# Kernel optimization log

Measured on AMD Instinct MI355X. Metric: run time of the kernel, lower is better.

## Reference

```python
import jax, jax.numpy as jnp
import numpy as np

B = 1024           # number of drug pairs (graphs per side)
ATOMS = 64         # atoms per molecule
N = B * ATOMS      # total atoms per side
H = 512            # hidden_size * number_of_molecules
FFN_H = 2048
OUT = 86           # num_tasks


def setup_inputs() -> dict:
    key = jax.random.key(0)
    ks = jax.random.split(key, 12)
    inv = 1.0 / np.sqrt(H)
    inv2 = 1.0 / np.sqrt(2 * H)
    invf = 1.0 / np.sqrt(FFN_H)
    return {
        "left_output": jax.random.normal(ks[0], (B, H), jnp.float32),
        "right_output": jax.random.normal(ks[1], (B, H), jnp.float32),
        "left_atom": jax.random.normal(ks[2], (N, H), jnp.float32),
        "right_atom": jax.random.normal(ks[3], (N, H), jnp.float32),
        "left_batch": jnp.arange(N, dtype=jnp.int32) // ATOMS,
        "right_batch": jnp.arange(N, dtype=jnp.int32) // ATOMS,
        "noise": jax.random.uniform(ks[4], (B, H), jnp.float32),
        "w_i_w": jax.random.normal(ks[5], (H, H), jnp.float32) * inv,
        "w_i_b": jnp.zeros((H,), jnp.float32),
        "prj_i_w": jax.random.normal(ks[6], (H, H), jnp.float32) * inv,
        "prj_i_b": jnp.zeros((H,), jnp.float32),
        "ffn1_w": jax.random.normal(ks[7], (2 * H, FFN_H), jnp.float32) * inv2,
        "ffn1_b": jnp.zeros((FFN_H,), jnp.float32),
        "ffn2_w": jax.random.normal(ks[8], (FFN_H, OUT), jnp.float32) * invf,
        "ffn2_b": jnp.zeros((OUT,), jnp.float32),
    }


def _seg_softmax(s, seg, num_segments):
    m = jax.ops.segment_max(s, seg, num_segments=num_segments)
    e = jnp.exp(s - m[seg])
    z = jax.ops.segment_sum(e, seg, num_segments=num_segments)
    return e / z[seg]


def reference(left_output, right_output, left_atom, right_atom,
              left_batch, right_batch, noise,
              w_i_w, w_i_b, prj_i_w, prj_i_b,
              ffn1_w, ffn1_b, ffn2_w, ffn2_b):
    # repeat_interleave(left_output, degree(right_batch)) == gather by segment id
    left_align = left_output[right_batch]    # [N_r, H]
    right_align = right_output[left_batch]   # [N_l, H]

    # cross-molecule coattention scores (elementwise product + reduce)
    left_scores = jnp.sum((left_atom @ w_i_w + w_i_b) * (right_align @ prj_i_w + prj_i_b), axis=-1)
    left_scores = _seg_softmax(left_scores, left_batch, B)
    right_scores = jnp.sum((right_atom @ w_i_w + w_i_b) * (left_align @ prj_i_w + prj_i_b), axis=-1)
    right_scores = _seg_softmax(right_scores, right_batch, B)

    # attention-weighted global add pool
    h_output = jax.ops.segment_sum(left_atom * right_align * left_scores[:, None], left_batch, num_segments=B)
    t_output = jax.ops.segment_sum(right_atom * left_align * right_scores[:, None], right_batch, num_segments=B)

    # sign-directed noise perturbation (same noise for both sides, as in original)
    nrm = jnp.maximum(jnp.linalg.norm(noise, axis=-1, keepdims=True), 1e-12)
    noise_n = noise / nrm
    h_pert = h_output + jnp.sign(h_output) * noise_n * 0.1
    t_pert = t_output + jnp.sign(t_output) * noise_n * 0.1

    pair = jnp.concatenate([h_pert, t_pert], axis=-1)  # [B, 2H]
    hid = jax.nn.relu(pair @ ffn1_w + ffn1_b)
    output = hid @ ffn2_w + ffn2_b  # training mode: raw logits, no sigmoid
    return (output, h_output, h_pert, left_scores, right_scores, left_output, right_output)
```

## Files before the change

### kernel.cpp

```cpp
#include <hip/hip_runtime.h>
#include <hip/hip_bf16.h>
#include <float.h>

#define B_ 1024
#define H_ 512
#define N_ (B_ * 64)
#define FFN_ 2048
#define OUT_ 86

typedef __bf16 bf16_t;
typedef __attribute__((ext_vector_type(8))) __bf16 bf16x8;
typedef __attribute__((ext_vector_type(4))) float f32x4;

__device__ __forceinline__ float wred_sum(float v) {
#pragma unroll
  for (int m = 32; m; m >>= 1) v += __shfl_xor(v, m);
  return v;
}

__device__ __forceinline__ void gload_lds16(const void* g, void* l) {
  __builtin_amdgcn_global_load_lds((const __attribute__((address_space(1))) unsigned int*)g,
                                   (__attribute__((address_space(3))) unsigned int*)l, 16, 0, 0);
}

template <bool BT, bool BIAS>
__global__ __launch_bounds__(256) void gemm64(const float* __restrict__ A1, const float* __restrict__ A2,
                                              int M1, const float* __restrict__ Bm,
                                              const float* __restrict__ bias, float* __restrict__ C,
                                              int N, int K) {
  __shared__ float As[16][68];
  __shared__ float Bs[16][68];
  const int bm = blockIdx.x * 64, bn = blockIdx.y * 64;
  const float* __restrict__ A = (bm < M1) ? (A1 + (size_t)bm * K) : (A2 + (size_t)(bm - M1) * K);
  const int t = threadIdx.x;
  const int tx = t & 15, ty = t >> 4;
  float acc[4][4] = {};
  for (int k0 = 0; k0 < K; k0 += 16) {
#pragma unroll
    for (int i = 0; i < 4; i++) {
      int m = (t >> 4) + i * 16;
      As[t & 15][m] = A[(size_t)m * K + k0 + (t & 15)];
    }
    if (BT) {
#pragma unroll
      for (int i = 0; i < 4; i++) {
        int n = (t >> 4) + i * 16;
        Bs[t & 15][n] = Bm[(size_t)(bn + n) * K + k0 + (t & 15)];
      }
    } else {
#pragma unroll
      for (int i = 0; i < 4; i++) {
        int kk = (t >> 6) + i * 4;
        Bs[kk][t & 63] = Bm[(size_t)(k0 + kk) * N + bn + (t & 63)];
      }
    }
    __syncthreads();
#pragma unroll
    for (int kk = 0; kk < 16; kk++) {
      float4 av = *(const float4*)&As[kk][ty * 4];
      float4 bv = *(const float4*)&Bs[kk][tx * 4];
      float a_[4] = {av.x, av.y, av.z, av.w};
      float b_[4] = {bv.x, bv.y, bv.z, bv.w};
#pragma unroll
      for (int i = 0; i < 4; i++)
#pragma unroll
        for (int j = 0; j < 4; j++) acc[i][j] += a_[i] * b_[j];
    }
    __syncthreads();
  }
#pragma unroll
  for (int i = 0; i < 4; i++) {
    int m = bm + ty * 4 + i;
    float tmp[4];
#pragma unroll
    for (int j = 0; j < 4; j++) {
      float x = acc[i][j];
      if (BIAS) x += bias[bn + tx * 4 + j];
      tmp[j] = x;
    }
    float4 v;
    v.x = tmp[0]; v.y = tmp[1]; v.z = tmp[2]; v.w = tmp[3];
    *(float4*)&C[(size_t)m * N + bn + tx * 4] = v;
  }
}

__global__ __launch_bounds__(256) void k_atoms6(const float* __restrict__ atomL, const float* __restrict__ atomR,
                                                const float* __restrict__ uLR,
                                                float* __restrict__ scoresL, float* __restrict__ scoresR,
                                                float* __restrict__ pL, float* __restrict__ pR) {
  const int pair = blockIdx.x;
  const int side = pair >> 10, b = pair & 1023;
  const int t = threadIdx.x, wave = t >> 6, lane = t & 63;

  __shared__ __align__(16) float sbuf[4][2][2][512];
  __shared__ float s_raw[64];
  __shared__ float mz[4][2];

  const float* __restrict__ atom = side ? atomR : atomL;
  const float* __restrict__ u = uLR + (size_t)pair * H_;
  float ur[8];
  *(f32x4*)&ur[0] = *(const f32x4*)&u[lane * 4];
  *(f32x4*)&ur[4] = *(const f32x4*)&u[256 + lane * 4];

  const char* gbase = (const char*)(atom + ((size_t)b * 64 + wave * 16) * H_);

  {
    char* lb = (char*)&sbuf[wave][0][0][0];
    gload_lds16(gbase + lane * 16, lb + lane * 16);
    gload_lds16(gbase + 1024 + lane * 16, lb + 1024 + lane * 16);
    gload_lds16(gbase + 2048 + lane * 16, lb + 2048 + lane * 16);
    gload_lds16(gbase + 3072 + lane * 16, lb + 3072 + lane * 16);
  }

  float q[8] = {};
  float m_run = -FLT_MAX, z_run = 0.f, myraw = 0.f;

#pragma unroll
  for (int c = 0; c < 8; c++) {
    if (c < 7) {
      const char* gb = gbase + (size_t)(c + 1) * 4096;
      char* lb = (char*)&sbuf[wave][(c + 1) & 1][0][0];
      gload_lds16(gb + lane * 16, lb + lane * 16);
      gload_lds16(gb + 1024 + lane * 16, lb + 1024 + lane * 16);
      gload_lds16(gb + 2048 + lane * 16, lb + 2048 + lane * 16);
      gload_lds16(gb + 3072 + lane * 16, lb + 3072 + lane * 16);
      asm volatile("s_waitcnt vmcnt(4)" ::: "memory");
    } else {
      asm volatile("s_waitcnt vmcnt(0)" ::: "memory");
    }
    __builtin_amdgcn_sched_barrier(0);
    const float* bc = &sbuf[wave][c & 1][0][0];
    float a0[8], a1[8];
    *(f32x4*)&a0[0] = *(const f32x4*)(bc + lane * 4);
    *(f32x4*)&a0[4] = *(const f32x4*)(bc + 256 + lane * 4);
    *(f32x4*)&a1[0] = *(const f32x4*)(bc + 512 + lane * 4);
    *(f32x4*)&a1[4] = *(const f32x4*)(bc + 512 + 256 + lane * 4);
    float d0 = 0.f, d1 = 0.f;
#pragma unroll
    for (int j = 0; j < 8; j++) { d0 += a0[j] * ur[j]; d1 += a1[j] * ur[j]; }
    d0 = wred_sum(d0);
    d1 = wred_sum(d1);
    myraw = (lane == wave * 16 + c * 2) ? d0 : myraw;
    myraw = (lane == wave * 16 + c * 2 + 1) ? d1 : myraw;
    float m_new = fmaxf(m_run, fmaxf(d0, d1));
    float r = __expf(m_run - m_new);
    float e0 = __expf(d0 - m_new), e1 = __expf(d1 - m_new);
    z_run = z_run * r + e0 + e1;
    m_run = m_new;
#pragma unroll
    for (int j = 0; j < 8; j++) q[j] = q[j] * r + e0 * a0[j] + e1 * a1[j];
  }

  if (lane == 0) { mz[wave][0] = m_run; mz[wave][1] = z_run; }
  if ((lane >> 4) == wave) s_raw[lane] = myraw;
  __syncthreads();

  const float M = fmaxf(fmaxf(mz[0][0], mz[1][0]), fmaxf(mz[2][0], mz[3][0]));
  const float Z = mz[0][1] * __expf(mz[0][0] - M) + mz[1][1] * __expf(mz[1][0] - M) +
                  mz[2][1] * __expf(mz[2][0] - M) + mz[3][1] * __expf(mz[3][0] - M);
  const float zinv = 1.f / Z;
  const float f = __expf(m_run - M);

  float* pp = &sbuf[0][0][0][0];
  f32x4 q0 = {q[0] * f, q[1] * f, q[2] * f, q[3] * f};
  f32x4 q1 = {q[4] * f, q[5] * f, q[6] * f, q[7] * f};
  *(f32x4*)&pp[wave * 512 + lane * 4] = q0;
  *(f32x4*)&pp[wave * 512 + 256 + lane * 4] = q1;
  __syncthreads();

  float v0 = (pp[t] + pp[512 + t] + pp[1024 + t] + pp[1536 + t]) * zinv;
  float v1 = (pp[t + 256] + pp[512 + t + 256] + pp[1024 + t + 256] + pp[1536 + t + 256]) * zinv;
  float* p = (side ? pR : pL) + (size_t)b * H_;
  p[t] = v0;
  p[t + 256] = v1;
  if (t < 64) (side ? scoresR : scoresL)[(size_t)b * 64 + t] = __expf(s_raw[t] - M) * zinv;
}

__global__ __launch_bounds__(512) void k_pert(const float* __restrict__ lo, const float* __restrict__ ro,
                                              const float* __restrict__ noise,
                                              const float* __restrict__ pL, const float* __restrict__ pR,
                                              float* __restrict__ h_out, float* __restrict__ h_pert,
                                              bf16_t* __restrict__ pairbf) {
  const int b = blockIdx.x, t = threadIdx.x;
  float nv = noise[(size_t)b * H_ + t];
  float sq = nv * nv;
  sq = wred_sum(sq);
  __shared__ float red[8];
  if ((t & 63) == 0) red[t >> 6] = sq;
  __syncthreads();
  float tot = 0.f;
#pragma unroll
  for (int i = 0; i < 8; i++) tot += red[i];
  float nrm = fmaxf(sqrtf(tot), 1e-12f);
  float nn = nv / nrm * 0.1f;
  float h = ro[(size_t)b * H_ + t] * pL[(size_t)b * H_ + t];
  float tt = lo[(size_t)b * H_ + t] * pR[(size_t)b * H_ + t];
  float sh = (h > 0.f) ? 1.f : ((h < 0.f) ? -1.f : 0.f);
  float st = (tt > 0.f) ? 1.f : ((tt < 0.f) ? -1.f : 0.f);
  float hp = h + sh * nn;
  float tp = tt + st * nn;
  h_out[(size_t)b * H_ + t] = h;
  h_pert[(size_t)b * H_ + t] = hp;
  pairbf[(size_t)b * 1024 + t] = (bf16_t)hp;
  pairbf[(size_t)b * 1024 + 512 + t] = (bf16_t)tp;
}

__global__ __launch_bounds__(256) void k_w1t(const float* __restrict__ W1, bf16_t* __restrict__ W1t) {
  __shared__ float tile[32][33];
  const int bx = blockIdx.x;
  const int by = blockIdx.y;
  const int tx = threadIdx.x & 31, ty = threadIdx.x >> 5;
#pragma unroll
  for (int i = ty; i < 32; i += 8)
    tile[i][tx] = W1[(size_t)(by * 32 + i) * FFN_ + bx * 32 + tx];
  __syncthreads();
#pragma unroll
  for (int i = ty; i < 32; i += 8)
    W1t[(size_t)(bx * 32 + i) * 1024 + by * 32 + tx] = (bf16_t)tile[tx][i];
}

__global__ __launch_bounds__(256) void k_ffn1(const bf16_t* __restrict__ Abf, const bf16_t* __restrict__ Bt,
                                              const float* __restrict__ bias, float* __restrict__ C) {
  __shared__ bf16_t As[64 * 64];
  __shared__ bf16_t Bs[64 * 64];
  const int bm = blockIdx.x * 64, bn = blockIdx.y * 64;
  const int t = threadIdx.x;
  const int lane = t & 63, wave = t >> 6;
  const int wm = wave & 1, wn = wave >> 1;
  const int l15 = lane & 15, l4 = lane >> 4;
  f32x4 acc[2][2] = {{{0.f, 0.f, 0.f, 0.f}, {0.f, 0.f, 0.f, 0.f}},
                     {{0.f, 0.f, 0.f, 0.f}, {0.f, 0.f, 0.f, 0.f}}};

  for (int k0 = 0; k0 < 1024; k0 += 64) {
#pragma unroll
    for (int r = 0; r < 2; r++) {
      const int off = (r * 256 + t) * 16;
      const int row = off >> 7;
      const int g = (off >> 4) & 7;
      const int scb = ((g ^ (row & 7)) << 4);
      gload_lds16((const char*)Abf + (size_t)(bm + row) * 2048 + k0 * 2 + scb, (char*)As + off);
      gload_lds16((const char*)Bt + (size_t)(bn + row) * 2048 + k0 * 2 + scb, (char*)Bs + off);
    }
    __syncthreads();
#pragma unroll
    for (int ks = 0; ks < 2; ks++) {
      const int ar0 = wm * 32 + l15, ar1 = ar0 + 16;
      const int br0 = wn * 32 + l15, br1 = br0 + 16;
      const int gA = ks * 4 + l4;
      bf16x8 a0 = *(const bf16x8*)((const char*)As + ar0 * 128 + ((gA ^ (ar0 & 7)) << 4));
      bf16x8 a1 = *(const bf16x8*)((const char*)As + ar1 * 128 + ((gA ^ (ar1 & 7)) << 4));
      bf16x8 b0 = *(const bf16x8*)((const char*)Bs + br0 * 128 + ((gA ^ (br0 & 7)) << 4));
      bf16x8 b1 = *(const bf16x8*)((const char*)Bs + br1 * 128 + ((gA ^ (br1 & 7)) << 4));
      acc[0][0] = __builtin_amdgcn_mfma_f32_16x16x32_bf16(a0, b0, acc[0][0], 0, 0, 0);
      acc[0][1] = __builtin_amdgcn_mfma_f32_16x16x32_bf16(a0, b1, acc[0][1], 0, 0, 0);
      acc[1][0] = __builtin_amdgcn_mfma_f32_16x16x32_bf16(a1, b0, acc[1][0], 0, 0, 0);
      acc[1][1] = __builtin_amdgcn_mfma_f32_16x16x32_bf16(a1, b1, acc[1][1], 0, 0, 0);
    }
    __syncthreads();
  }
#pragma unroll
  for (int mi = 0; mi < 2; mi++)
#pragma unroll
    for (int nj = 0; nj < 2; nj++)
#pragma unroll
      for (int r = 0; r < 4; r++) {
        const int m = bm + wm * 32 + mi * 16 + l4 * 4 + r;
        const int n = bn + wn * 32 + nj * 16 + l15;
        float v = acc[mi][nj][r] + bias[n];
        C[(size_t)m * FFN_ + n] = fmaxf(v, 0.f);
      }
}

__global__ void k_w2t(const float* __restrict__ W2, float* __restrict__ W2t) {
  int idx = blockIdx.x * 256 + threadIdx.x;
  if (idx < OUT_ * FFN_) {
    int n = idx / FFN_, k = idx % FFN_;
    W2t[idx] = W2[(size_t)k * OUT_ + n];
  }
}

__global__ __launch_bounds__(256) void k_ffn2(const float* __restrict__ hid, const float* __restrict__ W2t,
                                              const float* __restrict__ b2, float* __restrict__ out) {
  const int b0 = blockIdx.x * 2;
  const int t = threadIdx.x, wave = t >> 6, lane = t & 63;
  float4 h0[8], h1[8];
  const float* r0 = hid + (size_t)b0 * FFN_;
#pragma unroll
  for (int j = 0; j < 8; j++) {
    h0[j] = *(const float4*)&r0[lane * 4 + j * 256];
    h1[j] = *(const float4*)&r0[FFN_ + lane * 4 + j * 256];
  }
  for (int n = wave; n < OUT_; n += 4) {
    const float* wrow = W2t + (size_t)n * FFN_;
    float s0 = 0.f, s1 = 0.f;
#pragma unroll
    for (int j = 0; j < 8; j++) {
      float4 w4 = *(const float4*)&wrow[lane * 4 + j * 256];
      s0 += w4.x * h0[j].x + w4.y * h0[j].y + w4.z * h0[j].z + w4.w * h0[j].w;
      s1 += w4.x * h1[j].x + w4.y * h1[j].y + w4.z * h1[j].z + w4.w * h1[j].w;
    }
    s0 = wred_sum(s0);
    s1 = wred_sum(s1);
    if (lane == 0) {
      out[(size_t)b0 * OUT_ + n] = s0 + b2[n];
      out[(size_t)(b0 + 1) * OUT_ + n] = s1 + b2[n];
    }
  }
}

extern "C" void kernel_launch(void* const* d_in, const int* in_sizes, int n_in,
                              void* d_out, int out_size, void* d_ws, size_t ws_size,
                              hipStream_t stream) {
  const float* lo = (const float*)d_in[0];
  const float* ro = (const float*)d_in[1];
  const float* la = (const float*)d_in[2];
  const float* ra = (const float*)d_in[3];
  const float* noise = (const float*)d_in[6];
  const float* w_i_w = (const float*)d_in[7];
  const float* prj_w = (const float*)d_in[9];
  const float* prj_b = (const float*)d_in[10];
  const float* W1 = (const float*)d_in[11];
  const float* b1 = (const float*)d_in[12];
  const float* W2 = (const float*)d_in[13];
  const float* b2 = (const float*)d_in[14];

  float* out = (float*)d_out;
  float* o_logits = out;
  float* o_hout  = out + 88064;
  float* o_hpert = o_hout + 524288;
  float* o_ls    = o_hpert + 524288;
  float* o_rs    = o_ls + 65536;
  float* o_lo    = o_rs + 65536;
  float* o_ro    = o_lo + 524288;

  float* ws = (float*)d_ws;
  float* T    = ws; ws += 2048 * 512;
  float* uLR  = ws; ws += 2048 * 512;
  float* pL   = ws; ws += B_ * H_;
  float* pR   = ws; ws += B_ * H_;
  float* hid  = ws; ws += B_ * FFN_;
  float* W2t  = ws; ws += OUT_ * FFN_;
  bf16_t* pairbf = (bf16_t*)ws; ws += B_ * 1024 / 2;
  bf16_t* W1t    = (bf16_t*)ws; ws += FFN_ * 1024 / 2;

  gemm64<false, true><<<dim3(32, 8), 256, 0, stream>>>(ro, lo, 1024, prj_w, prj_b, T, 512, 512);
  gemm64<true, false><<<dim3(32, 8), 256, 0, stream>>>(T, T, 1 << 30, w_i_w, nullptr, uLR, 512, 512);
  k_w1t<<<dim3(64, 32), 256, 0, stream>>>(W1, W1t);
  k_atoms6<<<2048, 256, 0, stream>>>(la, ra, uLR, o_ls, o_rs, pL, pR);
  k_pert<<<1024, 512, 0, stream>>>(lo, ro, noise, pL, pR, o_hout, o_hpert, pairbf);
  k_ffn1<<<dim3(16, 32), 256, 0, stream>>>(pairbf, W1t, b1, hid);
  k_w2t<<<688, 256, 0, stream>>>(W2, W2t);
  k_ffn2<<<512, 256, 0, stream>>>(hid, W2t, b2, o_logits);
  hipMemcpyAsync(o_lo, lo, (size_t)B_ * H_ * 4, hipMemcpyDeviceToDevice, stream);
  hipMemcpyAsync(o_ro, ro, (size_t)B_ * H_ * 4, hipMemcpyDeviceToDevice, stream);
}
```

Before: 164.8 us.

## Precompute combined weight matrix and rewrite atom attention as two-pass kernel

The projection chain is reassociated: a 512x512 matrix from w_i_w and prj_w plus a bias vector is built once, and the pooled outputs are then multiplied by it in a single GEMM. This replaces two 1024-row GEMMs and drops the T buffer. The atom kernel is also rewritten. It no longer streams atoms through LDS with an online softmax. Instead it computes all 64 scores with direct global loads, runs a block-wide softmax, and then reads the atoms a second time to form the weighted sum. That second read doubles atom traffic, though the rows for a molecule may still be in cache.

New measurement: 200.1 us. 1.21x slower.

```diff
diff --git a/kernel.cpp b/kernel.cpp
--- a/kernel.cpp
+++ b/kernel.cpp
@@ -17,10 +17,24 @@
   for (int m = 32; m; m >>= 1) v += __shfl_xor(v, m);
   return v;
 }
+__device__ __forceinline__ float wred_max(float v) {
+#pragma unroll
+  for (int m = 32; m; m >>= 1) v = fmaxf(v, __shfl_xor(v, m));
+  return v;
+}
 
 __device__ __forceinline__ void gload_lds16(const void* g, void* l) {
   __builtin_amdgcn_global_load_lds((const __attribute__((address_space(1))) unsigned int*)g,
                                    (__attribute__((address_space(3))) unsigned int*)l, 16, 0, 0);
+}
+
+__global__ void k_prep(const float* __restrict__ w_i_w, const float* __restrict__ prj_b,
+                       float* __restrict__ dv) {
+  int k = blockIdx.x, l = threadIdx.x;
+  float s = 0.f;
+  for (int h = l; h < H_; h += 64) s += w_i_w[k * H_ + h] * prj_b[h];
+  s = wred_sum(s);
+  if (l == 0) dv[k] = s;
 }
 
 template <bool BT, bool BIAS>
@@ -84,7 +98,7 @@
   }
 }
 
-__global__ __launch_bounds__(256) void k_atoms6(const float* __restrict__ atomL, const float* __restrict__ atomR,
+__global__ __launch_bounds__(256) void k_atoms8(const float* __restrict__ atomL, const float* __restrict__ atomR,
                                                 const float* __restrict__ uLR,
                                                 float* __restrict__ scoresL, float* __restrict__ scoresR,
                                                 float* __restrict__ pL, float* __restrict__ pR) {
@@ -92,88 +106,56 @@
   const int side = pair >> 10, b = pair & 1023;
   const int t = threadIdx.x, wave = t >> 6, lane = t & 63;
 
-  __shared__ __align__(16) float sbuf[4][2][2][512];
-  __shared__ float s_raw[64];
-  __shared__ float mz[4][2];
+  __shared__ float s_all[64];
+  __shared__ float s_nrm[64];
 
   const float* __restrict__ atom = side ? atomR : atomL;
   const float* __restrict__ u = uLR + (size_t)pair * H_;
-  float ur[8];
-  *(f32x4*)&ur[0] = *(const f32x4*)&u[lane * 4];
-  *(f32x4*)&ur[4] = *(const f32x4*)&u[256 + lane * 4];
-
-  const char* gbase = (const char*)(atom + ((size_t)b * 64 + wave * 16) * H_);
-
-  {
-    char* lb = (char*)&sbuf[wave][0][0][0];
-    gload_lds16(gbase + lane * 16, lb + lane * 16);
-    gload_lds16(gbase + 1024 + lane * 16, lb + 1024 + lane * 16);
-    gload_lds16(gbase + 2048 + lane * 16, lb + 2048 + lane * 16);
-    gload_lds16(gbase + 3072 + lane * 16, lb + 3072 + lane * 16);
-  }
-
-  float q[8] = {};
-  float m_run = -FLT_MAX, z_run = 0.f, myraw = 0.f;
-
-#pragma unroll
-  for (int c = 0; c < 8; c++) {
-    if (c < 7) {
-      const char* gb = gbase + (size_t)(c + 1) * 4096;
-      char* lb = (char*)&sbuf[wave][(c + 1) & 1][0][0];
-      gload_lds16(gb + lane * 16, lb + lane * 16);
-      gload_lds16(gb + 1024 + lane * 16, lb + 1024 + lane * 16);
-      gload_lds16(gb + 2048 + lane * 16, lb + 2048 + lane * 16);
-      gload_lds16(gb + 3072 + lane * 16, lb + 3072 + lane * 16);
-      asm volatile("s_waitcnt vmcnt(4)" ::: "memory");
-    } else {
-      asm volatile("s_waitcnt vmcnt(0)" ::: "memory");
-    }
-    __builtin_amdgcn_sched_barrier(0);
-    const float* bc = &sbuf[wave][c & 1][0][0];
-    float a0[8], a1[8];
-    *(f32x4*)&a0[0] = *(const f32x4*)(bc + lane * 4);
-    *(f32x4*)&a0[4] = *(const f32x4*)(bc + 256 + lane * 4);
-    *(f32x4*)&a1[0] = *(const f32x4*)(bc + 512 + lane * 4);
-    *(f32x4*)&a1[4] = *(const f32x4*)(bc + 512 + 256 + lane * 4);
-    float d0 = 0.f, d1 = 0.f;
-#pragma unroll
-    for (int j = 0; j < 8; j++) { d0 += a0[j] * ur[j]; d1 += a1[j] * ur[j]; }
-    d0 = wred_sum(d0);
-    d1 = wred_sum(d1);
-    myraw = (lane == wave * 16 + c * 2) ? d0 : myraw;
-    myraw = (lane == wave * 16 + c * 2 + 1) ? d1 : myraw;
-    float m_new = fmaxf(m_run, fmaxf(d0, d1));
-    float r = __expf(m_run - m_new);
-    float e0 = __expf(d0 - m_new), e1 = __expf(d1 - m_new);
-    z_run = z_run * r + e0 + e1;
-    m_run = m_new;
-#pragma unroll
-    for (int j = 0; j < 8; j++) q[j] = q[j] * r + e0 * a0[j] + e1 * a1[j];
-  }
-
-  if (lane == 0) { mz[wave][0] = m_run; mz[wave][1] = z_run; }
-  if ((lane >> 4) == wave) s_raw[lane] = myraw;
+  f32x4 u0 = *(const f32x4*)&u[lane * 4];
+  f32x4 u1 = *(const f32x4*)&u[256 + lane * 4];
+
+  const float* __restrict__ base = atom + ((size_t)b * 64 + wave * 16) * H_;
+  float d[16];
+#pragma unroll
+  for (int i = 0; i < 16; i++) {
+    const float* rp = base + (size_t)i * H_;
+    f32x4 x0 = *(const f32x4*)(rp + lane * 4);
+    f32x4 x1 = *(const f32x4*)(rp + 256 + lane * 4);
+    d[i] = x0.x * u0.x + x0.y * u0.y + x0.z * u0.z + x0.w * u0.w +
+           x1.x * u1.x + x1.y * u1.y + x1.z * u1.z + x1.w * u1.w;
+  }
+#pragma unroll
+  for (int i = 0; i < 16; i++) d[i] = wred_sum(d[i]);
+  if (lane < 16) {
+    float myv = 0.f;
+#pragma unroll
+    for (int i = 0; i < 16; i++) myv = (lane == i) ? d[i] : myv;
+    s_all[wave * 16 + lane] = myv;
+  }
   __syncthreads();
 
-  const float M = fmaxf(fmaxf(mz[0][0], mz[1][0]), fmaxf(mz[2][0], mz[3][0]));
-  const float Z = mz[0][1] * __expf(mz[0][0] - M) + mz[1][1] * __expf(mz[1][0] - M) +
-                  mz[2][1] * __expf(mz[2][0] - M) + mz[3][1] * __expf(mz[3][0] - M);
-  const float zinv = 1.f / Z;
-  const float f = __expf(m_run - M);
-
-  float* pp = &sbuf[0][0][0][0];
-  f32x4 q0 = {q[0] * f, q[1] * f, q[2] * f, q[3] * f};
-  f32x4 q1 = {q[4] * f, q[5] * f, q[6] * f, q[7] * f};
-  *(f32x4*)&pp[wave * 512 + lane * 4] = q0;
-  *(f32x4*)&pp[wave * 512 + 256 + lane * 4] = q1;
+  float sv = s_all[lane];
+  float M = wred_max(sv);
+  float e = __expf(sv - M);
+  float Z = wred_sum(e);
+  float w_n = e / Z;
+  if (wave == 0) {
+    s_nrm[lane] = w_n;
+    (side ? scoresR : scoresL)[(size_t)b * 64 + lane] = w_n;
+  }
   __syncthreads();
 
-  float v0 = (pp[t] + pp[512 + t] + pp[1024 + t] + pp[1536 + t]) * zinv;
-  float v1 = (pp[t + 256] + pp[512 + t + 256] + pp[1024 + t + 256] + pp[1536 + t + 256]) * zinv;
+  const float* __restrict__ ab = atom + (size_t)b * 64 * H_;
+  float q0 = 0.f, q1 = 0.f;
+#pragma unroll 8
+  for (int r = 0; r < 64; r++) {
+    const float w = s_nrm[r];
+    q0 += w * ab[(size_t)r * H_ + t];
+    q1 += w * ab[(size_t)r * H_ + t + 256];
+  }
   float* p = (side ? pR : pL) + (size_t)b * H_;
-  p[t] = v0;
-  p[t + 256] = v1;
-  if (t < 64) (side ? scoresR : scoresL)[(size_t)b * 64 + t] = __expf(s_raw[t] - M) * zinv;
+  p[t] = q0;
+  p[t + 256] = q1;
 }
 
 __global__ __launch_bounds__(512) void k_pert(const float* __restrict__ lo, const float* __restrict__ ro,
@@ -334,7 +316,7 @@
   float* o_ro    = o_lo + 524288;
 
   float* ws = (float*)d_ws;
-  float* T    = ws; ws += 2048 * 512;
+  float* Mt   = ws; ws += 512 * 512;
   float* uLR  = ws; ws += 2048 * 512;
   float* pL   = ws; ws += B_ * H_;
   float* pR   = ws; ws += B_ * H_;
@@ -342,11 +324,13 @@
   float* W2t  = ws; ws += OUT_ * FFN_;
   bf16_t* pairbf = (bf16_t*)ws; ws += B_ * 1024 / 2;
   bf16_t* W1t    = (bf16_t*)ws; ws += FFN_ * 1024 / 2;
-
-  gemm64<false, true><<<dim3(32, 8), 256, 0, stream>>>(ro, lo, 1024, prj_w, prj_b, T, 512, 512);
-  gemm64<true, false><<<dim3(32, 8), 256, 0, stream>>>(T, T, 1 << 30, w_i_w, nullptr, uLR, 512, 512);
+  float* dv   = ws; ws += 512;
+
+  k_prep<<<512, 64, 0, stream>>>(w_i_w, prj_b, dv);
+  gemm64<true, false><<<dim3(8, 8), 256, 0, stream>>>(w_i_w, w_i_w, 1 << 30, prj_w, nullptr, Mt, 512, 512);
+  gemm64<true, true><<<dim3(32, 8), 256, 0, stream>>>(ro, lo, 1024, Mt, dv, uLR, 512, 512);
   k_w1t<<<dim3(64, 32), 256, 0, stream>>>(W1, W1t);
-  k_atoms6<<<2048, 256, 0, stream>>>(la, ra, uLR, o_ls, o_rs, pL, pR);
+  k_atoms8<<<2048, 256, 0, stream>>>(la, ra, uLR, o_ls, o_rs, pL, pR);
   k_pert<<<1024, 512, 0, stream>>>(lo, ro, noise, pL, pR, o_hout, o_hpert, pairbf);
   k_ffn1<<<dim3(16, 32), 256, 0, stream>>>(pairbf, W1t, b1, hid);
   k_w2t<<<688, 256, 0, stream>>>(W2, W2t);
```
